# Kernel tuning notes

Measured on AMD Instinct MI355X. Metric: run time of the kernel, lower is better.

## Reference

```python
import jax, jax.numpy as jnp
import numpy as np
from jax import lax

# Static config (mirrors Caps2dMatwo init_kwargs)
K_SIZE = 5
T1 = 8              # num_capsule (output capsule types)
POS = (4, 4)
APP = (4, 4)
ROUTINGS = 3
COORD_ADD = True
ZP = POS[0] * POS[1]   # 16
ZA = APP[0] * APP[1]   # 16
Z = ZP + ZA            # 32 == input channels z_0


def _psquash(p, axis):
    return p / jnp.max(jnp.abs(p), axis=axis, keepdims=True)


def _matwo_squash(p, axis):
    n2 = jnp.sum(p * p, axis=axis, keepdims=True)
    n = jnp.sqrt(n2 + 1e-9)
    return n2 / (1.0 + n2) * p / n


def _coord_const(H, W):
    # coordinate_addition: adds normalized (x, y) into last row of the pos matrix
    yy, xx = np.meshgrid(np.arange(H), np.arange(W), indexing='ij')
    c = np.zeros((H * W, 1, POS[1], POS[1]), np.float32)
    c[:, 0, -1, 0] = xx.reshape(-1) / W
    c[:, 0, -1, 1] = yy.reshape(-1) / H
    return jnp.asarray(c)


def setup_inputs() -> dict:
    key = jax.random.key(0)
    k1, k2, k3, k4, k5 = jax.random.split(key, 5)
    N, T0, H, W = 4, 4, 96, 96
    return {
        'input_tensor': jax.random.normal(k1, (N, T0, Z, H, W), jnp.float32),
        'W_conv': jax.random.normal(k2, (T0, K_SIZE, K_SIZE, 1, T1), jnp.float32) * 0.05,
        'W_pos': jax.random.normal(k3, (T0, POS[1] * POS[1], T1), jnp.float32) * 0.05,
        'W_app': jax.random.normal(k4, (T0, APP[1] * APP[1], T1), jnp.float32) * 0.05,
        'b_app': jax.random.normal(k5, (T0, T1), jnp.float32) * 0.05,
    }


def reference(input_tensor, W_conv, W_pos, W_app, b_app):
    N, t0, z0, H, W = input_tensor.shape
    coord = _coord_const(H, W)
    u_hat_list = []
    for i in range(t0):
        # per input capsule type: spatial conv applied channel-wise
        u_t = input_tensor[:, i].reshape(N * z0, H, W, 1)
        u_spat = lax.conv_general_dilated(
            u_t, W_conv[i], (1, 1), 'SAME',
            dimension_numbers=('NHWC', 'HWIO', 'NHWC'))        # [N*z0, H, W, T1]
        u_spat = (u_spat.reshape(N, z0, H, W, T1)
                  .transpose(0, 2, 3, 4, 1)                    # [N,H,W,T1,z0]
                  .reshape(N, H, W, T1 * z0))
        u_pos = u_spat[..., :T1 * ZP].reshape(N, H, W, T1, POS[0], POS[1])
        u_app = u_spat[..., T1 * ZP:].reshape(N, H, W, T1, APP[0], APP[1])
        m_pos = W_pos[i].reshape(T1, POS[1], POS[1])
        m_app = W_app[i].reshape(T1, APP[1], APP[1])
        u_app = u_app + b_app[i].reshape(1, 1, 1, T1, 1, 1)
        # l2 normalize pos matrix along axis -2 (tf.l2_normalize semantics)
        m_pos = m_pos / jnp.sqrt(jnp.maximum(
            jnp.sum(m_pos * m_pos, axis=-2, keepdims=True), 1e-12))
        if COORD_ADD:
            m_pos = (m_pos + coord).reshape(1, H, W, T1, POS[1], POS[1])
        # matmult2d == batched matmul
        u_hat_pos = jnp.matmul(u_pos, m_pos).reshape(N, H, W, T1, ZP)
        u_hat_app = jnp.matmul(u_app, m_app).reshape(N, H, W, T1, ZA)
        u_hat_t = jnp.concatenate([u_hat_pos, u_hat_app], axis=-1)
        u_hat_list.append(u_hat_t.transpose(0, 4, 1, 2, 3))    # [N,Z,H,W,T1]
    u_hat = jnp.stack(u_hat_list, axis=-2)                     # [N,Z,H,W,t0,T1]

    # dual routing (sigmoid agreement), vectorized across output capsules
    u_pos_all = u_hat[:, :ZP]
    u_app_all = u_hat[:, ZP:]
    b = jnp.zeros((N, H, W, t0, T1), input_tensor.dtype)
    for _ in range(ROUTINGS - 1):
        r = jax.nn.sigmoid(b)                                  # [N,H,W,t0,T1]
        p = jnp.einsum('nzhwot,nhwot->tnzhw', u_hat, r)        # [T1,N,Z,H,W]
        v_pos = _psquash(p[:, :, :ZP], 2)
        v_app = _matwo_squash(p[:, :, ZP:], 2)
        rout = (jnp.einsum('nzhwot,tnzhw->nhwot', u_pos_all, v_pos)
                * jnp.einsum('nzhwot,tnzhw->nhwot', u_app_all, v_app))
        b = b + rout
    c = jax.nn.sigmoid(b)

    p = jnp.einsum('nzhwot,nhwot->tnzhw', u_hat, c)
    v_pos = _psquash(p[:, :, :ZP], 2)
    v_app = _matwo_squash(p[:, :, ZP:], 2)
    out = jnp.concatenate([v_pos, v_app], axis=2)              # [T1,N,Z,H,W]
    return out.transpose(1, 0, 2, 3, 4)                        # [N,T1,Z,H,W]
```

## Files before the change

### kernel.cpp

```cpp
#include <hip/hip_runtime.h>
#include <hip/hip_fp16.h>
#include <math.h>

#define IMG_H 96
#define IMG_W 96
#define HW (IMG_H * IMG_W)
#define TW 16
#define TH 4
#define TR (TH + 4)
#define TC 20
#define TS2 36

__device__ __forceinline__ float quad_sum(float v) {
    v += __int_as_float(__builtin_amdgcn_update_dpp(
            0, __float_as_int(v), 0xB1, 0xF, 0xF, true));
    v += __int_as_float(__builtin_amdgcn_update_dpp(
            0, __float_as_int(v), 0x4E, 0xF, 0xF, true));
    return v;
}
__device__ __forceinline__ float quad_max(float v) {
    v = fmaxf(v, __int_as_float(__builtin_amdgcn_update_dpp(
            0, __float_as_int(v), 0xB1, 0xF, 0xF, true)));
    v = fmaxf(v, __int_as_float(__builtin_amdgcn_update_dpp(
            0, __float_as_int(v), 0x4E, 0xF, 0xF, true)));
    return v;
}

__device__ __forceinline__ void route_store(const float (*uh)[8], int q, int nt,
                                            int pix, float* __restrict__ out)
{
    float bb[4] = {0.0f, 0.0f, 0.0f, 0.0f};
    #pragma unroll
    for (int it = 0; it < 2; ++it) {
        float r0 = 1.0f / (1.0f + __expf(-bb[0]));
        float r1 = 1.0f / (1.0f + __expf(-bb[1]));
        float r2 = 1.0f / (1.0f + __expf(-bb[2]));
        float r3 = 1.0f / (1.0f + __expf(-bb[3]));
        float pz[4], pa[4];
        #pragma unroll
        for (int j = 0; j < 4; ++j)
            pz[j] = fmaf(uh[0][j], r0, fmaf(uh[1][j], r1,
                    fmaf(uh[2][j], r2, uh[3][j] * r3)));
        float mx = quad_max(fmaxf(fmaxf(fabsf(pz[0]), fabsf(pz[1])),
                                  fmaxf(fabsf(pz[2]), fabsf(pz[3]))));
        float dp[4];
        #pragma unroll
        for (int o = 0; o < 4; ++o)
            dp[o] = quad_sum(fmaf(uh[o][0], pz[0], fmaf(uh[o][1], pz[1],
                             fmaf(uh[o][2], pz[2], uh[o][3] * pz[3]))));
        #pragma unroll
        for (int j = 0; j < 4; ++j)
            pa[j] = fmaf(uh[0][4 + j], r0, fmaf(uh[1][4 + j], r1,
                    fmaf(uh[2][4 + j], r2, uh[3][4 + j] * r3)));
        float n2 = quad_sum(fmaf(pa[0], pa[0], fmaf(pa[1], pa[1],
                            fmaf(pa[2], pa[2], pa[3] * pa[3]))));
        float invm = 1.0f / mx;
        float sc   = n2 / ((1.0f + n2) * sqrtf(n2 + 1e-9f));
        #pragma unroll
        for (int o = 0; o < 4; ++o) {
            float da = quad_sum(fmaf(uh[o][4], pa[0], fmaf(uh[o][5], pa[1],
                               fmaf(uh[o][6], pa[2], uh[o][7] * pa[3]))));
            bb[o] += (invm * dp[o]) * (sc * da);
        }
    }
    float r0 = 1.0f / (1.0f + __expf(-bb[0]));
    float r1 = 1.0f / (1.0f + __expf(-bb[1]));
    float r2 = 1.0f / (1.0f + __expf(-bb[2]));
    float r3 = 1.0f / (1.0f + __expf(-bb[3]));
    float pz[4], pa[4];
    #pragma unroll
    for (int j = 0; j < 4; ++j)
        pz[j] = fmaf(uh[0][j], r0, fmaf(uh[1][j], r1,
                fmaf(uh[2][j], r2, uh[3][j] * r3)));
    float mx = quad_max(fmaxf(fmaxf(fabsf(pz[0]), fabsf(pz[1])),
                              fmaxf(fabsf(pz[2]), fabsf(pz[3]))));
    #pragma unroll
    for (int j = 0; j < 4; ++j)
        pa[j] = fmaf(uh[0][4 + j], r0, fmaf(uh[1][4 + j], r1,
                fmaf(uh[2][4 + j], r2, uh[3][4 + j] * r3)));
    float n2 = quad_sum(fmaf(pa[0], pa[0], fmaf(pa[1], pa[1],
                        fmaf(pa[2], pa[2], pa[3] * pa[3]))));
    float invm = 1.0f / mx;
    float sc   = n2 / ((1.0f + n2) * sqrtf(n2 + 1e-9f));
    float* op = out + ((size_t)nt * 32 + (q << 2)) * HW + pix;
    op[0 * HW] = pz[0] * invm;
    op[1 * HW] = pz[1] * invm;
    op[2 * HW] = pz[2] * invm;
    op[3 * HW] = pz[3] * invm;
    op[16 * HW] = pa[0] * sc;
    op[17 * HW] = pa[1] * sc;
    op[18 * HW] = pa[2] * sc;
    op[19 * HW] = pa[3] * sc;
}

__global__ void __launch_bounds__(1024, 8)
caps_one_kernel(const float* __restrict__ x,
                const float* __restrict__ Wc,
                const float* __restrict__ Wp,
                const float* __restrict__ Wa,
                const float* __restrict__ Ba,
                float* __restrict__ out)
{
    __shared__ __align__(16) __half2 tile2[TR * TC * TS2];
    __shared__ __align__(16) __half2 wpk[400];
    __shared__ __align__(16) float   msh[512];
    __shared__ __align__(16) float   ash[512];

    const int tid    = threadIdx.x;
    const int q      = tid & 3;
    const int px     = (tid >> 2) & 15;
    const int wv     = tid >> 6;
    const int rr     = wv >> 2;
    const int wb     = blockIdx.x * TW;
    const int h0     = blockIdx.y * TH;
    const int n      = blockIdx.z >> 1;
    const int parity = blockIdx.z & 1;
    const int t      = parity + 2 * (wv & 3);
    const int w      = wb + px;
    const int h      = h0 + rr;

    if (tid < 400) {
        int i   = tid;
        int fp  = i / 100;
        int rem = i - fp * 100;
        int tap = rem >> 2;
        int g   = i & 3;
        int oe  = (g & 1) << 1;
        int f   = fp + ((g >> 1) << 2);
        wpk[i] = __floats2half2_rn(Wc[oe * 200 + tap * 8 + f],
                                   Wc[(oe + 1) * 200 + tap * 8 + f]);
    }
    if (tid >= 512 && tid < 640) {
        int j  = tid - 512;
        int c  = j & 3;
        int tt = (j >> 2) & 7;
        int oo = j >> 5;
        const float* src = Wp + oo * 128 + tt * 16 + c;
        float v0 = src[0], v1 = src[4], v2 = src[8], v3 = src[12];
        float s = v0 * v0 + v1 * v1 + v2 * v2 + v3 * v3;
        float inv = 1.0f / sqrtf(fmaxf(s, 1e-12f));
        float* dst = msh + (oo * 8 + tt) * 16 + c;
        dst[0] = v0 * inv; dst[4] = v1 * inv; dst[8] = v2 * inv; dst[12] = v3 * inv;
    } else if (tid >= 640 && tid < 768) {
        int i = tid - 640;
        ((float4*)ash)[i] = ((const float4*)Wa)[i];
    }
    {
        const int col = tid & 15;
        const int g   = tid >> 4;
        const int dy    = g >> 3;
        const int cpg   = g & 7;
        const int hh    = h0 + dy - 2;
        const int zq    = cpg >> 1;
        const int cbase = (cpg & 1) << 1;
        const int chan  = n * 128 + parity * 16 + zq * 4 + cbase;
        float v[8];
        #pragma unroll
        for (int j = 0; j < 8; ++j) v[j] = 0.0f;
        if ((unsigned)hh < IMG_H) {
            const float* src = x + (size_t)chan * HW + hh * IMG_W + wb + col;
            #pragma unroll
            for (int j = 0; j < 8; ++j)
                v[j] = src[(size_t)((j & 3) * 32 + (j >> 2)) * HW];
        }
        __half2 h4[4];
        #pragma unroll
        for (int j = 0; j < 4; ++j)
            h4[j] = __floats2half2_rn(v[2 * j], v[2 * j + 1]);
        *(uint4*)&tile2[(dy * TC + 2 + col) * TS2 + (cpg << 2)] =
            *(const uint4*)h4;

        const int m  = tid & 3;
        const int xx = (m < 2) ? m : (m + TW);
        const int ww = wb - 2 + xx;
        const int rh = tid >> 2;
        const int hdy = rh >> 5;
        const int cp  = rh & 31;
        const int hhh = h0 + hdy - 2;
        const int o0  = (cp & 1) << 1;
        const int hc  = (cp >> 1) & 3;
        const int hzq = cp >> 3;
        const int hchan = n * 128 + o0 * 32 + parity * 16 + hzq * 4 + hc;
        float v0 = 0.0f, v1 = 0.0f;
        if ((unsigned)hhh < IMG_H && (unsigned)ww < IMG_W) {
            const float* src = x + (size_t)hchan * HW + hhh * IMG_W + ww;
            v0 = src[0];
            v1 = src[(size_t)32 * HW];
        }
        tile2[(hdy * TC + xx) * TS2 + cp] = __floats2half2_rn(v0, v1);
    }
    __syncthreads();

    __half2 rp2[8], ra2[8];
    const __half2 z2 = __float2half2_rn(0.0f);
    #pragma unroll
    for (int i = 0; i < 8; ++i) { rp2[i] = z2; ra2[i] = z2; }

    const uint4* wb4 = (const uint4*)&wpk[(t >> 1) * 100];
    #pragma unroll
    for (int dy = 0; dy < 5; ++dy) {
        #pragma unroll
        for (int dx = 0; dx < 5; ++dx) {
            const __half2* t2 =
                &tile2[((rr + dy) * TC + px + dx) * TS2 + (q << 3)];
            union { uint4 u; __half2 hh[4]; } A, B, Wt;
            A.u  = *(const uint4*)t2;
            B.u  = *(const uint4*)(t2 + 4);
            Wt.u = wb4[dy * 5 + dx];
            rp2[0] = __hfma2(A.hh[0], Wt.hh[0], rp2[0]);
            rp2[1] = __hfma2(A.hh[1], Wt.hh[1], rp2[1]);
            rp2[2] = __hfma2(A.hh[2], Wt.hh[0], rp2[2]);
            rp2[3] = __hfma2(A.hh[3], Wt.hh[1], rp2[3]);
            rp2[4] = __hfma2(B.hh[0], Wt.hh[0], rp2[4]);
            rp2[5] = __hfma2(B.hh[1], Wt.hh[1], rp2[5]);
            rp2[6] = __hfma2(B.hh[2], Wt.hh[0], rp2[6]);
            rp2[7] = __hfma2(B.hh[3], Wt.hh[1], rp2[7]);
            ra2[0] = __hfma2(A.hh[0], Wt.hh[2], ra2[0]);
            ra2[1] = __hfma2(A.hh[1], Wt.hh[3], ra2[1]);
            ra2[2] = __hfma2(A.hh[2], Wt.hh[2], ra2[2]);
            ra2[3] = __hfma2(A.hh[3], Wt.hh[3], ra2[3]);
            ra2[4] = __hfma2(B.hh[0], Wt.hh[2], ra2[4]);
            ra2[5] = __hfma2(B.hh[1], Wt.hh[3], ra2[5]);
            ra2[6] = __hfma2(B.hh[2], Wt.hh[2], ra2[6]);
            ra2[7] = __hfma2(B.hh[3], Wt.hh[3], ra2[7]);
        }
    }

    float uh[4][8];
    {
        const float cx = (float)w * (1.0f / 96.0f);
        const float cy = (float)h * (1.0f / 96.0f);
        #pragma unroll
        for (int o = 0; o < 4; ++o) {
            const float* mb = &msh[(o * 8 + t) * 16];
            float4 m0 = *(const float4*)(mb + 0);
            float4 m1 = *(const float4*)(mb + 4);
            float4 m2 = *(const float4*)(mb + 8);
            float4 m3 = *(const float4*)(mb + 12);
            m3.x += cx;
            m3.y += cy;
            const int pr = o >> 1;
            float r0, r1, r2, r3;
            if (o & 1) {
                r0 = __high2float(rp2[0 + pr]); r1 = __high2float(rp2[2 + pr]);
                r2 = __high2float(rp2[4 + pr]); r3 = __high2float(rp2[6 + pr]);
            } else {
                r0 = __low2float(rp2[0 + pr]);  r1 = __low2float(rp2[2 + pr]);
                r2 = __low2float(rp2[4 + pr]);  r3 = __low2float(rp2[6 + pr]);
            }
            uh[o][0] = r0 * m0.x + r1 * m1.x + r2 * m2.x + r3 * m3.x;
            uh[o][1] = r0 * m0.y + r1 * m1.y + r2 * m2.y + r3 * m3.y;
            uh[o][2] = r0 * m0.z + r1 * m1.z + r2 * m2.z + r3 * m3.z;
            uh[o][3] = r0 * m0.w + r1 * m1.w + r2 * m2.w + r3 * m3.w;
        }
        #pragma unroll
        for (int o = 0; o < 4; ++o) {
            const float* ab = &ash[(o * 8 + t) * 16];
            float4 a0 = *(const float4*)(ab + 0);
            float4 a1 = *(const float4*)(ab + 4);
            float4 a2 = *(const float4*)(ab + 8);
            float4 a3 = *(const float4*)(ab + 12);
            const float bias = Ba[o * 8 + t];
            const int pr = o >> 1;
            float r0, r1, r2, r3;
            if (o & 1) {
                r0 = __high2float(ra2[0 + pr]); r1 = __high2float(ra2[2 + pr]);
                r2 = __high2float(ra2[4 + pr]); r3 = __high2float(ra2[6 + pr]);
            } else {
                r0 = __low2float(ra2[0 + pr]);  r1 = __low2float(ra2[2 + pr]);
                r2 = __low2float(ra2[4 + pr]);  r3 = __low2float(ra2[6 + pr]);
            }
            r0 += bias; r1 += bias; r2 += bias; r3 += bias;
            uh[o][4] = r0 * a0.x + r1 * a1.x + r2 * a2.x + r3 * a3.x;
            uh[o][5] = r0 * a0.y + r1 * a1.y + r2 * a2.y + r3 * a3.y;
            uh[o][6] = r0 * a0.z + r1 * a1.z + r2 * a2.z + r3 * a3.z;
            uh[o][7] = r0 * a0.w + r1 * a1.w + r2 * a2.w + r3 * a3.w;
        }
    }

    route_store(uh, q, n * 8 + t, h * IMG_W + w, out);
}

extern "C" void kernel_launch(void* const* d_in, const int* in_sizes, int n_in,
                              void* d_out, int out_size, void* d_ws, size_t ws_size,
                              hipStream_t stream) {
    const float* x  = (const float*)d_in[0];
    const float* Wc = (const float*)d_in[1];
    const float* Wp = (const float*)d_in[2];
    const float* Wa = (const float*)d_in[3];
    const float* Ba = (const float*)d_in[4];
    float* outp = (float*)d_out;

    caps_one_kernel<<<dim3(IMG_W / TW, IMG_H / TH, 8), 1024, 0, stream>>>(
        x, Wc, Wp, Wa, Ba, outp);
}
```

Before: 123.9 us.

## Compute two output capsule types per thread and halve block size

```diff
diff --git a/kernel.cpp b/kernel.cpp
--- a/kernel.cpp
+++ b/kernel.cpp
@@ -93,7 +93,63 @@
     op[19 * HW] = pa[3] * sc;
 }
 
-__global__ void __launch_bounds__(1024, 8)
+__device__ __forceinline__ void emit_route(
+    const __half2* rp2, const __half2* ra2,
+    const float* msh, const float* ash, const float* __restrict__ Ba,
+    int t, int q, int nt, int pix, float cx, float cy,
+    float* __restrict__ out)
+{
+    float uh[4][8];
+    #pragma unroll
+    for (int o = 0; o < 4; ++o) {
+        const float* mb = &msh[(o * 8 + t) * 16];
+        float4 m0 = *(const float4*)(mb + 0);
+        float4 m1 = *(const float4*)(mb + 4);
+        float4 m2 = *(const float4*)(mb + 8);
+        float4 m3 = *(const float4*)(mb + 12);
+        m3.x += cx;
+        m3.y += cy;
+        const int pr = o >> 1;
+        float r0, r1, r2, r3;
+        if (o & 1) {
+            r0 = __high2float(rp2[0 + pr]); r1 = __high2float(rp2[2 + pr]);
+            r2 = __high2float(rp2[4 + pr]); r3 = __high2float(rp2[6 + pr]);
+        } else {
+            r0 = __low2float(rp2[0 + pr]);  r1 = __low2float(rp2[2 + pr]);
+            r2 = __low2float(rp2[4 + pr]);  r3 = __low2float(rp2[6 + pr]);
+        }
+        uh[o][0] = r0 * m0.x + r1 * m1.x + r2 * m2.x + r3 * m3.x;
+        uh[o][1] = r0 * m0.y + r1 * m1.y + r2 * m2.y + r3 * m3.y;
+        uh[o][2] = r0 * m0.z + r1 * m1.z + r2 * m2.z + r3 * m3.z;
+        uh[o][3] = r0 * m0.w + r1 * m1.w + r2 * m2.w + r3 * m3.w;
+    }
+    #pragma unroll
+    for (int o = 0; o < 4; ++o) {
+        const float* ab = &ash[(o * 8 + t) * 16];
+        float4 a0 = *(const float4*)(ab + 0);
+        float4 a1 = *(const float4*)(ab + 4);
+        float4 a2 = *(const float4*)(ab + 8);
+        float4 a3 = *(const float4*)(ab + 12);
+        const float bias = Ba[o * 8 + t];
+        const int pr = o >> 1;
+        float r0, r1, r2, r3;
+        if (o & 1) {
+            r0 = __high2float(ra2[0 + pr]); r1 = __high2float(ra2[2 + pr]);
+            r2 = __high2float(ra2[4 + pr]); r3 = __high2float(ra2[6 + pr]);
+        } else {
+            r0 = __low2float(ra2[0 + pr]);  r1 = __low2float(ra2[2 + pr]);
+            r2 = __low2float(ra2[4 + pr]);  r3 = __low2float(ra2[6 + pr]);
+        }
+        r0 += bias; r1 += bias; r2 += bias; r3 += bias;
+        uh[o][4] = r0 * a0.x + r1 * a1.x + r2 * a2.x + r3 * a3.x;
+        uh[o][5] = r0 * a0.y + r1 * a1.y + r2 * a2.y + r3 * a3.y;
+        uh[o][6] = r0 * a0.z + r1 * a1.z + r2 * a2.z + r3 * a3.z;
+        uh[o][7] = r0 * a0.w + r1 * a1.w + r2 * a2.w + r3 * a3.w;
+    }
+    route_store(uh, q, nt, pix, out);
+}
+
+__global__ void __launch_bounds__(512)
 caps_one_kernel(const float* __restrict__ x,
                 const float* __restrict__ Wc,
                 const float* __restrict__ Wp,
@@ -110,12 +166,15 @@
     const int q      = tid & 3;
     const int px     = (tid >> 2) & 15;
     const int wv     = tid >> 6;
-    const int rr     = wv >> 2;
+    const int rr     = wv >> 1;
+    const int sa     = (wv & 1) << 1;
+    const int sb     = sa + 1;
     const int wb     = blockIdx.x * TW;
     const int h0     = blockIdx.y * TH;
     const int n      = blockIdx.z >> 1;
     const int parity = blockIdx.z & 1;
-    const int t      = parity + 2 * (wv & 3);
+    const int ta     = parity + 2 * sa;
+    const int tb     = parity + 2 * sb;
     const int w      = wb + px;
     const int h      = h0 + rr;
 
@@ -130,8 +189,12 @@
         wpk[i] = __floats2half2_rn(Wc[oe * 200 + tap * 8 + f],
                                    Wc[(oe + 1) * 200 + tap * 8 + f]);
     }
-    if (tid >= 512 && tid < 640) {
-        int j  = tid - 512;
+    if (tid >= 256 && tid < 384) {
+        int i = tid - 256;
+        ((float4*)ash)[i] = ((const float4*)Wa)[i];
+    }
+    if (tid >= 384) {
+        int j  = tid - 384;
         int c  = j & 3;
         int tt = (j >> 2) & 7;
         int oo = j >> 5;
@@ -141,144 +204,117 @@
         float inv = 1.0f / sqrtf(fmaxf(s, 1e-12f));
         float* dst = msh + (oo * 8 + tt) * 16 + c;
         dst[0] = v0 * inv; dst[4] = v1 * inv; dst[8] = v2 * inv; dst[12] = v3 * inv;
-    } else if (tid >= 640 && tid < 768) {
-        int i = tid - 640;
-        ((float4*)ash)[i] = ((const float4*)Wa)[i];
     }
     {
         const int col = tid & 15;
-        const int g   = tid >> 4;
-        const int dy    = g >> 3;
-        const int cpg   = g & 7;
-        const int hh    = h0 + dy - 2;
-        const int zq    = cpg >> 1;
-        const int cbase = (cpg & 1) << 1;
-        const int chan  = n * 128 + parity * 16 + zq * 4 + cbase;
-        float v[8];
-        #pragma unroll
-        for (int j = 0; j < 8; ++j) v[j] = 0.0f;
-        if ((unsigned)hh < IMG_H) {
-            const float* src = x + (size_t)chan * HW + hh * IMG_W + wb + col;
+        #pragma unroll
+        for (int k = 0; k < 2; ++k) {
+            const int g     = (tid >> 4) + (k << 5);
+            const int dy    = g >> 3;
+            const int cpg   = g & 7;
+            const int hh    = h0 + dy - 2;
+            const int zq    = cpg >> 1;
+            const int cbase = (cpg & 1) << 1;
+            const int chan  = n * 128 + parity * 16 + zq * 4 + cbase;
+            float v[8];
             #pragma unroll
-            for (int j = 0; j < 8; ++j)
-                v[j] = src[(size_t)((j & 3) * 32 + (j >> 2)) * HW];
-        }
-        __half2 h4[4];
-        #pragma unroll
-        for (int j = 0; j < 4; ++j)
-            h4[j] = __floats2half2_rn(v[2 * j], v[2 * j + 1]);
-        *(uint4*)&tile2[(dy * TC + 2 + col) * TS2 + (cpg << 2)] =
-            *(const uint4*)h4;
-
+            for (int j = 0; j < 8; ++j) v[j] = 0.0f;
+            if ((unsigned)hh < IMG_H) {
+                const float* src = x + (size_t)chan * HW + hh * IMG_W + wb + col;
+                #pragma unroll
+                for (int j = 0; j < 8; ++j)
+                    v[j] = src[(size_t)((j & 3) * 32 + (j >> 2)) * HW];
+            }
+            __half2 h4[4];
+            #pragma unroll
+            for (int j = 0; j < 4; ++j)
+                h4[j] = __floats2half2_rn(v[2 * j], v[2 * j + 1]);
+            *(uint4*)&tile2[(dy * TC + 2 + col) * TS2 + (cpg << 2)] =
+                *(const uint4*)h4;
+        }
         const int m  = tid & 3;
         const int xx = (m < 2) ? m : (m + TW);
         const int ww = wb - 2 + xx;
-        const int rh = tid >> 2;
-        const int hdy = rh >> 5;
-        const int cp  = rh & 31;
-        const int hhh = h0 + hdy - 2;
-        const int o0  = (cp & 1) << 1;
-        const int hc  = (cp >> 1) & 3;
-        const int hzq = cp >> 3;
-        const int hchan = n * 128 + o0 * 32 + parity * 16 + hzq * 4 + hc;
-        float v0 = 0.0f, v1 = 0.0f;
-        if ((unsigned)hhh < IMG_H && (unsigned)ww < IMG_W) {
-            const float* src = x + (size_t)hchan * HW + hhh * IMG_W + ww;
-            v0 = src[0];
-            v1 = src[(size_t)32 * HW];
-        }
-        tile2[(hdy * TC + xx) * TS2 + cp] = __floats2half2_rn(v0, v1);
+        #pragma unroll
+        for (int k = 0; k < 2; ++k) {
+            const int rh  = (tid >> 2) + (k << 7);
+            const int hdy = rh >> 5;
+            const int cp  = rh & 31;
+            const int hhh = h0 + hdy - 2;
+            const int o0  = (cp & 1) << 1;
+            const int hc  = (cp >> 1) & 3;
+            const int hzq = cp >> 3;
+            const int hchan = n * 128 + o0 * 32 + parity * 16 + hzq * 4 + hc;
+            float v0 = 0.0f, v1 = 0.0f;
+            if ((unsigned)hhh < IMG_H && (unsigned)ww < IMG_W) {
+                const float* src = x + (size_t)hchan * HW + hhh * IMG_W + ww;
+                v0 = src[0];
+                v1 = src[(size_t)32 * HW];
+            }
+            tile2[(hdy * TC + xx) * TS2 + cp] = __floats2half2_rn(v0, v1);
+        }
     }
     __syncthreads();
 
-    __half2 rp2[8], ra2[8];
+    __half2 rpa[8], raa[8], rpb[8], rab[8];
     const __half2 z2 = __float2half2_rn(0.0f);
     #pragma unroll
-    for (int i = 0; i < 8; ++i) { rp2[i] = z2; ra2[i] = z2; }
-
-    const uint4* wb4 = (const uint4*)&wpk[(t >> 1) * 100];
+    for (int i = 0; i < 8; ++i) { rpa[i] = z2; raa[i] = z2; rpb[i] = z2; rab[i] = z2; }
+
+    const uint4* wb4a = (const uint4*)&wpk[sa * 100];
+    const uint4* wb4b = (const uint4*)&wpk[sb * 100];
     #pragma unroll
     for (int dy = 0; dy < 5; ++dy) {
         #pragma unroll
         for (int dx = 0; dx < 5; ++dx) {
             const __half2* t2 =
                 &tile2[((rr + dy) * TC + px + dx) * TS2 + (q << 3)];
-            union { uint4 u; __half2 hh[4]; } A, B, Wt;
-            A.u  = *(const uint4*)t2;
-            B.u  = *(const uint4*)(t2 + 4);
-            Wt.u = wb4[dy * 5 + dx];
-            rp2[0] = __hfma2(A.hh[0], Wt.hh[0], rp2[0]);
-            rp2[1] = __hfma2(A.hh[1], Wt.hh[1], rp2[1]);
-            rp2[2] = __hfma2(A.hh[2], Wt.hh[0], rp2[2]);
-            rp2[3] = __hfma2(A.hh[3], Wt.hh[1], rp2[3]);
-            rp2[4] = __hfma2(B.hh[0], Wt.hh[0], rp2[4]);
-            rp2[5] = __hfma2(B.hh[1], Wt.hh[1], rp2[5]);
-            rp2[6] = __hfma2(B.hh[2], Wt.hh[0], rp2[6]);
-            rp2[7] = __hfma2(B.hh[3], Wt.hh[1], rp2[7]);
-            ra2[0] = __hfma2(A.hh[0], Wt.hh[2], ra2[0]);
-            ra2[1] = __hfma2(A.hh[1], Wt.hh[3], ra2[1]);
-            ra2[2] = __hfma2(A.hh[2], Wt.hh[2], ra2[2]);
-            ra2[3] = __hfma2(A.hh[3], Wt.hh[3], ra2[3]);
-            ra2[4] = __hfma2(B.hh[0], Wt.hh[2], ra2[4]);
-            ra2[5] = __hfma2(B.hh[1], Wt.hh[3], ra2[5]);
-            ra2[6] = __hfma2(B.hh[2], Wt.hh[2], ra2[6]);
-            ra2[7] = __hfma2(B.hh[3], Wt.hh[3], ra2[7]);
-        }
-    }
-
-    float uh[4][8];
-    {
-        const float cx = (float)w * (1.0f / 96.0f);
-        const float cy = (float)h * (1.0f / 96.0f);
-        #pragma unroll
-        for (int o = 0; o < 4; ++o) {
-            const float* mb = &msh[(o * 8 + t) * 16];
-            float4 m0 = *(const float4*)(mb + 0);
-            float4 m1 = *(const float4*)(mb + 4);
-            float4 m2 = *(const float4*)(mb + 8);
-            float4 m3 = *(const float4*)(mb + 12);
-            m3.x += cx;
-            m3.y += cy;
-            const int pr = o >> 1;
-            float r0, r1, r2, r3;
-            if (o & 1) {
-                r0 = __high2float(rp2[0 + pr]); r1 = __high2float(rp2[2 + pr]);
-                r2 = __high2float(rp2[4 + pr]); r3 = __high2float(rp2[6 + pr]);
-            } else {
-                r0 = __low2float(rp2[0 + pr]);  r1 = __low2float(rp2[2 + pr]);
-                r2 = __low2float(rp2[4 + pr]);  r3 = __low2float(rp2[6 + pr]);
-            }
-            uh[o][0] = r0 * m0.x + r1 * m1.x + r2 * m2.x + r3 * m3.x;
-            uh[o][1] = r0 * m0.y + r1 * m1.y + r2 * m2.y + r3 * m3.y;
-            uh[o][2] = r0 * m0.z + r1 * m1.z + r2 * m2.z + r3 * m3.z;
-            uh[o][3] = r0 * m0.w + r1 * m1.w + r2 * m2.w + r3 * m3.w;
-        }
-        #pragma unroll
-        for (int o = 0; o < 4; ++o) {
-            const float* ab = &ash[(o * 8 + t) * 16];
-            float4 a0 = *(const float4*)(ab + 0);
-            float4 a1 = *(const float4*)(ab + 4);
-            float4 a2 = *(const float4*)(ab + 8);
-            float4 a3 = *(const float4*)(ab + 12);
-            const float bias = Ba[o * 8 + t];
-            const int pr = o >> 1;
-            float r0, r1, r2, r3;
-            if (o & 1) {
-                r0 = __high2float(ra2[0 + pr]); r1 = __high2float(ra2[2 + pr]);
-                r2 = __high2float(ra2[4 + pr]); r3 = __high2float(ra2[6 + pr]);
-            } else {
-                r0 = __low2float(ra2[0 + pr]);  r1 = __low2float(ra2[2 + pr]);
-                r2 = __low2float(ra2[4 + pr]);  r3 = __low2float(ra2[6 + pr]);
-            }
-            r0 += bias; r1 += bias; r2 += bias; r3 += bias;
-            uh[o][4] = r0 * a0.x + r1 * a1.x + r2 * a2.x + r3 * a3.x;
-            uh[o][5] = r0 * a0.y + r1 * a1.y + r2 * a2.y + r3 * a3.y;
-            uh[o][6] = r0 * a0.z + r1 * a1.z + r2 * a2.z + r3 * a3.z;
-            uh[o][7] = r0 * a0.w + r1 * a1.w + r2 * a2.w + r3 * a3.w;
-        }
-    }
-
-    route_store(uh, q, n * 8 + t, h * IMG_W + w, out);
+            union { uint4 u; __half2 hh[4]; } A, B, Wta, Wtb;
+            A.u   = *(const uint4*)t2;
+            B.u   = *(const uint4*)(t2 + 4);
+            Wta.u = wb4a[dy * 5 + dx];
+            Wtb.u = wb4b[dy * 5 + dx];
+            rpa[0] = __hfma2(A.hh[0], Wta.hh[0], rpa[0]);
+            rpa[1] = __hfma2(A.hh[1], Wta.hh[1], rpa[1]);
+            rpa[2] = __hfma2(A.hh[2], Wta.hh[0], rpa[2]);
+            rpa[3] = __hfma2(A.hh[3], Wta.hh[1], rpa[3]);
+            rpa[4] = __hfma2(B.hh[0], Wta.hh[0], rpa[4]);
+            rpa[5] = __hfma2(B.hh[1], Wta.hh[1], rpa[5]);
+            rpa[6] = __hfma2(B.hh[2], Wta.hh[0], rpa[6]);
+            rpa[7] = __hfma2(B.hh[3], Wta.hh[1], rpa[7]);
+            raa[0] = __hfma2(A.hh[0], Wta.hh[2], raa[0]);
+            raa[1] = __hfma2(A.hh[1], Wta.hh[3], raa[1]);
+            raa[2] = __hfma2(A.hh[2], Wta.hh[2], raa[2]);
+            raa[3] = __hfma2(A.hh[3], Wta.hh[3], raa[3]);
+            raa[4] = __hfma2(B.hh[0], Wta.hh[2], raa[4]);
+            raa[5] = __hfma2(B.hh[1], Wta.hh[3], raa[5]);
+            raa[6] = __hfma2(B.hh[2], Wta.hh[2], raa[6]);
+            raa[7] = __hfma2(B.hh[3], Wta.hh[3], raa[7]);
+            rpb[0] = __hfma2(A.hh[0], Wtb.hh[0], rpb[0]);
+            rpb[1] = __hfma2(A.hh[1], Wtb.hh[1], rpb[1]);
+            rpb[2] = __hfma2(A.hh[2], Wtb.hh[0], rpb[2]);
+            rpb[3] = __hfma2(A.hh[3], Wtb.hh[1], rpb[3]);
+            rpb[4] = __hfma2(B.hh[0], Wtb.hh[0], rpb[4]);
+            rpb[5] = __hfma2(B.hh[1], Wtb.hh[1], rpb[5]);
+            rpb[6] = __hfma2(B.hh[2], Wtb.hh[0], rpb[6]);
+            rpb[7] = __hfma2(B.hh[3], Wtb.hh[1], rpb[7]);
+            rab[0] = __hfma2(A.hh[0], Wtb.hh[2], rab[0]);
+            rab[1] = __hfma2(A.hh[1], Wtb.hh[3], rab[1]);
+            rab[2] = __hfma2(A.hh[2], Wtb.hh[2], rab[2]);
+            rab[3] = __hfma2(A.hh[3], Wtb.hh[3], rab[3]);
+            rab[4] = __hfma2(B.hh[0], Wtb.hh[2], rab[4]);
+            rab[5] = __hfma2(B.hh[1], Wtb.hh[3], rab[5]);
+            rab[6] = __hfma2(B.hh[2], Wtb.hh[2], rab[6]);
+            rab[7] = __hfma2(B.hh[3], Wtb.hh[3], rab[7]);
+        }
+    }
+
+    const float cx = (float)w * (1.0f / 96.0f);
+    const float cy = (float)h * (1.0f / 96.0f);
+    const int pix = h * IMG_W + w;
+
+    emit_route(rpa, raa, msh, ash, Ba, ta, q, n * 8 + ta, pix, cx, cy, out);
+    emit_route(rpb, rab, msh, ash, Ba, tb, q, n * 8 + tb, pix, cx, cy, out);
 }
 
 extern "C" void kernel_launch(void* const* d_in, const int* in_sizes, int n_in,
@@ -291,6 +327,6 @@
     const float* Ba = (const float*)d_in[4];
     float* outp = (float*)d_out;
 
-    caps_one_kernel<<<dim3(IMG_W / TW, IMG_H / TH, 8), 1024, 0, stream>>>(
+    caps_one_kernel<<<dim3(IMG_W / TW, IMG_H / TH, 8), 512, 0, stream>>>(
         x, Wc, Wp, Wa, Ba, outp);
 }
```

Measured after the change: 127.6 us. 1.03x slower.
